# Performance work log

Hardware: AMD Instinct MI355X
Metric: run time of the kernel (lower is better)

Reference implementation:

```python
import jax, jax.numpy as jnp
import numpy as np

NUM_LEVELS = 16
FEATS_PER_LEVEL = 2
LOG2_HASHMAP = 19
TABLE_SIZE = 1 << LOG2_HASHMAP
BASE_RES = 16
DESIRED_RES = 4096
PER_LEVEL_SCALE = float(np.exp(np.log(DESIRED_RES / BASE_RES) / (NUM_LEVELS - 1)))
PRIMES = (np.uint32(1), np.uint32(2654435761), np.uint32(805459861))
N_POINTS = 2_000_000


def _level_features(x, table, level):
    # x: [N,3] in [0,1]; table: [TABLE_SIZE, F]
    scale = BASE_RES * (PER_LEVEL_SCALE ** level) - 1.0
    res = int(np.ceil(scale)) + 1
    dense = (res ** 3) <= TABLE_SIZE  # tcnn uses dense indexing when grid fits
    pos = x * scale + 0.5
    pos0 = jnp.floor(pos)
    w = pos - pos0                     # trilinear weights, [N,3]
    base = pos0.astype(jnp.uint32)
    out = jnp.zeros((x.shape[0], table.shape[1]), dtype=table.dtype)
    for c in range(8):                 # 8 corners of the voxel
        offs = [(c >> d) & 1 for d in range(3)]
        pc = [jnp.minimum(base[:, d] + np.uint32(offs[d]), np.uint32(res - 1)) for d in range(3)]
        if dense:
            idx = pc[0] + pc[1] * np.uint32(res) + pc[2] * np.uint32(res * res)
        else:
            idx = (pc[0] * PRIMES[0]) ^ (pc[1] * PRIMES[1]) ^ (pc[2] * PRIMES[2])
            idx = idx & np.uint32(TABLE_SIZE - 1)
        wt = jnp.ones(x.shape[0], dtype=x.dtype)
        for d in range(3):
            wt = wt * (w[:, d] if offs[d] else (1.0 - w[:, d]))
        out = out + wt[:, None] * table[idx.astype(jnp.int32)]
    return out


def hashgrid_encode(x, tables):
    # x: [N,3] in [0,1]; tables: [L, TABLE_SIZE, F] -> [N, L*F]
    return jnp.concatenate(
        [_level_features(x, tables[l], l) for l in range(NUM_LEVELS)], axis=-1)


def setup_inputs() -> dict:
    key = jax.random.key(0)
    k1, k2, k3, k4, k5 = jax.random.split(key, 5)
    points = jax.random.uniform(k1, (N_POINTS, 3), dtype=jnp.float32)
    # tcnn hashgrid init: uniform(-1e-4, 1e-4)
    tables = jax.random.uniform(k2, (NUM_LEVELS, TABLE_SIZE, FEATS_PER_LEVEL),
                                minval=-1e-4, maxval=1e-4, dtype=jnp.float32)
    def kaiming(k, fan_out, fan_in):
        bound = np.sqrt(2.0) * np.sqrt(3.0 / fan_in)
        return jax.random.uniform(k, (fan_out, fan_in), minval=-bound, maxval=bound,
                                  dtype=jnp.float32)
    W1 = kaiming(k3, 32, 32)
    W2 = kaiming(k4, 32, 32)
    W3 = kaiming(k5, 4, 32)
    aabb = jnp.stack([jnp.zeros(3, jnp.float32), jnp.ones(3, jnp.float32)])
    return {"points": points, "tables": tables, "W1": W1, "W2": W2, "W3": W3,
            "aabb": aabb}


def reference(points, tables, W1, W2, W3, aabb):
    texc = jnp.clip((points - aabb[0][None, :]) / (aabb[1] - aabb[0])[None, :], 0.0, 1.0)
    enc = hashgrid_encode(texc, tables)            # [N, 32]
    h = jax.nn.relu(enc @ W1.T)
    h = jax.nn.relu(h @ W2.T)
    out = h @ W3.T                                 # [N, 4]
    mn = jnp.array([0.0, 0.0, 0.0, 0.01], dtype=out.dtype)
    mx = jnp.array([1.0, 1.0, 1.0, 1.0], dtype=out.dtype)
    return jax.nn.sigmoid(out) * (mx - mn) + mn
```

## Files before the change

kernel.cpp:

```cpp
#include <hip/hip_runtime.h>
#include <cmath>


namespace {
constexpr int kLevels = 16;
constexpr unsigned kTableSize = 1u << 19;
constexpr unsigned kMask = kTableSize - 1u;
constexpr int kCells = 262144;
constexpr int kScanBlocks = 256;

typedef _Float16 half2_t __attribute__((ext_vector_type(2)));
typedef unsigned int u32;

struct LevelParams {
  float scale[kLevels];
  unsigned res[kLevels];
  int dense[kLevels];
  unsigned toff[kLevels];
  unsigned cnt[kLevels];
};
}

__global__ __launch_bounds__(256)
void conv_tables_kernel(const float2* __restrict__ src, u32* __restrict__ dst,
                        LevelParams lp,
                        const float* __restrict__ W1, const float* __restrict__ W2,
                        const float* __restrict__ W3, half2_t* __restrict__ Wh,
                        u32* __restrict__ hist0)
{
  int gid = blockIdx.x * blockDim.x + threadIdx.x;
  if (gid < 512) {
    Wh[gid] = half2_t{(_Float16)W1[2 * gid], (_Float16)W1[2 * gid + 1]};
  } else if (gid < 1024) {
    int t = gid - 512;
    Wh[512 + t] = half2_t{(_Float16)W2[2 * t], (_Float16)W2[2 * t + 1]};
  } else if (gid < 1088) {
    int t = gid - 1024;
    Wh[1024 + t] = half2_t{(_Float16)W3[2 * t], (_Float16)W3[2 * t + 1]};
  }
  if (hist0 && gid < kCells) hist0[gid] = 0u;
  int l = blockIdx.x >> 11;
  unsigned e = (unsigned)((blockIdx.x & 2047) * blockDim.x + threadIdx.x);
  if (l < kLevels && e < lp.cnt[l]) {
    float2 v = src[(size_t)l * kTableSize + e];
    dst[lp.toff[l] + e] =
        __builtin_bit_cast(u32, half2_t{(_Float16)v.x, (_Float16)v.y});
  }
}

__device__ __forceinline__ void texc_of(const float* __restrict__ pts,
                                        const float* __restrict__ aabb, int i,
                                        float& x, float& y, float& z)
{
  float a0x = aabb[0], a0y = aabb[1], a0z = aabb[2];
  float a1x = aabb[3], a1y = aabb[4], a1z = aabb[5];
  x = fminf(fmaxf((pts[3 * i + 0] - a0x) / (a1x - a0x), 0.f), 1.f);
  y = fminf(fmaxf((pts[3 * i + 1] - a0y) / (a1y - a0y), 0.f), 1.f);
  z = fminf(fmaxf((pts[3 * i + 2] - a0z) / (a1z - a0z), 0.f), 1.f);
}

__device__ __forceinline__ u32 cell_of(float x, float y, float z)
{
  int cx = min((int)(x * 64.f), 63);
  int cy = min((int)(y * 64.f), 63);
  int cz = min((int)(z * 64.f), 63);
  return (u32)(cx + (cy << 6) + (cz << 12));
}

__global__ __launch_bounds__(256)
void hist_kernel(const float* __restrict__ points, const float* __restrict__ aabb,
                 u32* __restrict__ hist, int n)
{
  int i = blockIdx.x * blockDim.x + threadIdx.x;
  if (i >= n) return;
  float x, y, z;
  texc_of(points, aabb, i, x, y, z);
  atomicAdd(&hist[cell_of(x, y, z)], 1u);
}

__global__ __launch_bounds__(1024)
void scanA_kernel(u32* __restrict__ hist, u32* __restrict__ btot)
{
  __shared__ u32 sm[1024];
  int t = threadIdx.x;
  int i = (blockIdx.x << 10) + t;
  u32 x = hist[i];
  sm[t] = x;
  __syncthreads();
  u32 v = x;
  for (int off = 1; off < 1024; off <<= 1) {
    u32 a = (t >= off) ? sm[t - off] : 0u;
    __syncthreads();
    v += a;
    sm[t] = v;
    __syncthreads();
  }
  hist[i] = v - x;
  if (t == 1023) btot[blockIdx.x] = v;
}

__global__ __launch_bounds__(256)
void scatter_kernel(const float* __restrict__ points, const float* __restrict__ aabb,
                    u32* __restrict__ hist, const u32* __restrict__ btot,
                    float4* __restrict__ sorted, u32* __restrict__ perm, int n)
{
  __shared__ u32 bb[kScanBlocks];
  int t = threadIdx.x;
  u32 xv = btot[t];
  bb[t] = xv;
  __syncthreads();
  u32 v = xv;
  for (int off = 1; off < 256; off <<= 1) {
    u32 a = (t >= off) ? bb[t - off] : 0u;
    __syncthreads();
    v += a;
    bb[t] = v;
    __syncthreads();
  }
  u32 excl = v - xv;
  __syncthreads();
  bb[t] = excl;
  __syncthreads();

  int i = blockIdx.x * 256 + t;
  if (i >= n) return;
  float x, y, z;
  texc_of(points, aabb, i, x, y, z);
  u32 c = cell_of(x, y, z);
  u32 slot = bb[c >> 10] + atomicAdd(&hist[c], 1u);
  sorted[slot] = float4{x, y, z, 0.f};
  perm[slot] = (u32)i;
}

__device__ __forceinline__ u32 sel4(uint4 v, u32 j) {
  u32 lo = (j & 1u) ? v.y : v.x;
  u32 hi = (j & 1u) ? v.w : v.z;
  return (j & 2u) ? hi : lo;
}

__device__ __forceinline__ float dot2_acc(half2_t a, half2_t b, float c) {
#if __has_builtin(__builtin_amdgcn_fdot2)
  return __builtin_amdgcn_fdot2(a, b, c, false);
#else
  return c + (float)a.x * (float)b.x + (float)a.y * (float)b.y;
#endif
}

__device__ __forceinline__ u32 encode_level(float x, float y, float z,
                                            float s, unsigned res, bool dense,
                                            const u32* __restrict__ tab)
{
  unsigned rm1 = res - 1u;
  unsigned res2 = res * res;
  float fx = x * s + 0.5f, fy = y * s + 0.5f, fz = z * s + 0.5f;
  float fx0 = floorf(fx), fy0 = floorf(fy), fz0 = floorf(fz);
  float wx = fx - fx0, wy = fy - fy0, wz = fz - fz0;
  unsigned bx = (unsigned)fx0, by = (unsigned)fy0, bz = (unsigned)fz0;
  unsigned pcx0 = min(bx, rm1), pcx1 = min(bx + 1u, rm1);

  u32 idx0[4], idx1[4];
  #pragma unroll
  for (int q = 0; q < 4; ++q) {
    unsigned oy = (unsigned)(q & 1);
    unsigned oz = (unsigned)(q >> 1);
    unsigned pcy = min(by + oy, rm1);
    unsigned pcz = min(bz + oz, rm1);
    if (dense) {
      u32 b = pcy * res + pcz * res2;
      idx0[q] = pcx0 + b;
      idx1[q] = pcx1 + b;
    } else {
      u32 h = (pcy * 2654435761u) ^ (pcz * 805459861u);
      idx0[q] = (pcx0 ^ h) & kMask;
      idx1[q] = (pcx1 ^ h) & kMask;
    }
  }
  uint4 v[4];
  #pragma unroll
  for (int q = 0; q < 4; ++q)
    v[q] = *reinterpret_cast<const uint4*>(tab + (idx0[q] & ~3u));
  u32 e1x[4] = {0u, 0u, 0u, 0u};
  #pragma unroll
  for (int q = 0; q < 4; ++q) {
    if ((idx0[q] ^ idx1[q]) >= 4u) e1x[q] = tab[idx1[q]];
  }
  float wx1 = wx, wx0 = 1.f - wx;
  float acc0 = 0.f, acc1 = 0.f;
  #pragma unroll
  for (int q = 0; q < 4; ++q) {
    unsigned oy = (unsigned)(q & 1);
    unsigned oz = (unsigned)(q >> 1);
    float wyz = (oy ? wy : 1.f - wy) * (oz ? wz : 1.f - wz);
    u32 e0 = sel4(v[q], idx0[q] & 3u);
    u32 e1g = sel4(v[q], idx1[q] & 3u);
    u32 e1 = ((idx0[q] ^ idx1[q]) < 4u) ? e1g : e1x[q];
    half2_t f0 = __builtin_bit_cast(half2_t, e0);
    half2_t f1 = __builtin_bit_cast(half2_t, e1);
    float w0 = wyz * wx0, w1 = wyz * wx1;
    acc0 += w0 * (float)f0.x + w1 * (float)f1.x;
    acc1 += w0 * (float)f0.y + w1 * (float)f1.y;
  }
  return __builtin_bit_cast(u32, half2_t{(_Float16)acc0, (_Float16)acc1});
}

__global__ __launch_bounds__(256)
void encode_dense_kernel(const float4* __restrict__ pts,
                         const u32* __restrict__ tables,
                         u32* __restrict__ enc,
                         LevelParams lp, int nd, int n)
{
  int i = blockIdx.x * blockDim.x + threadIdx.x;
  if (i >= n) return;
  float4 p = pts[i];
  #pragma unroll 1
  for (int l = 0; l < nd; ++l) {
    enc[(size_t)l * n + i] = encode_level(p.x, p.y, p.z, lp.scale[l], lp.res[l],
                                          lp.dense[l] != 0, tables + lp.toff[l]);
  }
}

__global__ __launch_bounds__(256)
void encode_level_kernel(const float4* __restrict__ pts,
                         const u32* __restrict__ tables,
                         u32* __restrict__ enc,
                         LevelParams lp, int l, int n)
{
  int i = blockIdx.x * blockDim.x + threadIdx.x;
  if (i >= n) return;
  float4 p = pts[i];
  enc[(size_t)l * n + i] = encode_level(p.x, p.y, p.z, lp.scale[l], lp.res[l],
                                        lp.dense[l] != 0, tables + lp.toff[l]);
}

__global__ __launch_bounds__(256)
void encode_raw_kernel(const float* __restrict__ points,
                       const u32* __restrict__ tables,
                       const float* __restrict__ aabb,
                       u32* __restrict__ enc,
                       LevelParams lp, int n, int bpl)
{
  int l = blockIdx.x / bpl;
  int i = (blockIdx.x - l * bpl) * blockDim.x + threadIdx.x;
  if (i >= n) return;
  float x, y, z;
  texc_of(points, aabb, i, x, y, z);
  enc[(size_t)l * n + i] = encode_level(x, y, z, lp.scale[l], lp.res[l],
                                        lp.dense[l] != 0, tables + lp.toff[l]);
}

__global__ __launch_bounds__(256)
void mlp_kernel(const u32* __restrict__ enc,
                const half2_t* __restrict__ Wh,
                const u32* __restrict__ perm,
                float* __restrict__ out, int n)
{
  int i = blockIdx.x * blockDim.x + threadIdx.x;
  if (i >= n) return;

  u32 orig = perm ? perm[i] : (u32)i;

  half2_t e[16];
  #pragma unroll
  for (int l = 0; l < kLevels; ++l)
    e[l] = __builtin_bit_cast(half2_t, enc[(size_t)l * n + i]);

  const half2_t* W1h = Wh;
  const half2_t* W2h = Wh + 512;
  const half2_t* W3h = Wh + 1024;

  half2_t h1[16];
  #pragma unroll
  for (int jj = 0; jj < 16; ++jj) {
    float a0 = 0.f, a1 = 0.f;
    #pragma unroll
    for (int k = 0; k < 16; ++k) {
      a0 = dot2_acc(e[k], W1h[16 * (2 * jj) + k], a0);
      a1 = dot2_acc(e[k], W1h[16 * (2 * jj + 1) + k], a1);
    }
    h1[jj] = half2_t{(_Float16)fmaxf(a0, 0.f), (_Float16)fmaxf(a1, 0.f)};
  }

  half2_t h2[16];
  #pragma unroll
  for (int jj = 0; jj < 16; ++jj) {
    float a0 = 0.f, a1 = 0.f;
    #pragma unroll
    for (int k = 0; k < 16; ++k) {
      a0 = dot2_acc(h1[k], W2h[16 * (2 * jj) + k], a0);
      a1 = dot2_acc(h1[k], W2h[16 * (2 * jj + 1) + k], a1);
    }
    h2[jj] = half2_t{(_Float16)fmaxf(a0, 0.f), (_Float16)fmaxf(a1, 0.f)};
  }

  float o[4];
  #pragma unroll
  for (int j = 0; j < 4; ++j) {
    float acc = 0.f;
    #pragma unroll
    for (int k = 0; k < 16; ++k) acc = dot2_acc(h2[k], W3h[16 * j + k], acc);
    o[j] = acc;
  }

  float4 r;
  r.x = 1.f / (1.f + __expf(-o[0]));
  r.y = 1.f / (1.f + __expf(-o[1]));
  r.z = 1.f / (1.f + __expf(-o[2]));
  r.w = 0.99f / (1.f + __expf(-o[3])) + 0.01f;
  reinterpret_cast<float4*>(out)[orig] = r;
}

__global__ __launch_bounds__(256)
void hashgrid_mlp_kernel(const float* __restrict__ points,
                         const float* __restrict__ tables,
                         const float* __restrict__ W1,
                         const float* __restrict__ W2,
                         const float* __restrict__ W3,
                         const float* __restrict__ aabb,
                         float* __restrict__ out,
                         LevelParams lp, int n)
{
  int i = blockIdx.x * blockDim.x + threadIdx.x;
  if (i >= n) return;
  float x, y, z;
  texc_of(points, aabb, i, x, y, z);
  float enc[2 * kLevels];
  #pragma unroll
  for (int l = 0; l < kLevels; ++l) {
    float s = lp.scale[l];
    unsigned res = lp.res[l];
    bool dense = (lp.dense[l] != 0);
    unsigned rm1 = res - 1u;
    unsigned res2 = res * res;
    float fx = x * s + 0.5f, fy = y * s + 0.5f, fz = z * s + 0.5f;
    float fx0 = floorf(fx), fy0 = floorf(fy), fz0 = floorf(fz);
    float wx = fx - fx0, wy = fy - fy0, wz = fz - fz0;
    unsigned bx = (unsigned)fx0, by = (unsigned)fy0, bz = (unsigned)fz0;
    const float2* tab = reinterpret_cast<const float2*>(tables) + (size_t)l * kTableSize;
    float acc0 = 0.f, acc1 = 0.f;
    #pragma unroll
    for (int c = 0; c < 8; ++c) {
      unsigned ox = (unsigned)(c & 1);
      unsigned oy = (unsigned)((c >> 1) & 1);
      unsigned oz = (unsigned)((c >> 2) & 1);
      unsigned pcx = min(bx + ox, rm1);
      unsigned pcy = min(by + oy, rm1);
      unsigned pcz = min(bz + oz, rm1);
      unsigned idx;
      if (dense) idx = pcx + pcy * res + pcz * res2;
      else idx = (pcx ^ (pcy * 2654435761u) ^ (pcz * 805459861u)) & kMask;
      float wt = (ox ? wx : 1.f - wx) * (oy ? wy : 1.f - wy) * (oz ? wz : 1.f - wz);
      float2 f = tab[idx];
      acc0 += wt * f.x;
      acc1 += wt * f.y;
    }
    enc[2 * l + 0] = acc0;
    enc[2 * l + 1] = acc1;
  }
  float h1[32];
  #pragma unroll
  for (int j = 0; j < 32; ++j) {
    float acc = 0.f;
    #pragma unroll
    for (int k = 0; k < 32; ++k) acc += enc[k] * W1[32 * j + k];
    h1[j] = fmaxf(acc, 0.f);
  }
  float h2[32];
  #pragma unroll
  for (int j = 0; j < 32; ++j) {
    float acc = 0.f;
    #pragma unroll
    for (int k = 0; k < 32; ++k) acc += h1[k] * W2[32 * j + k];
    h2[j] = fmaxf(acc, 0.f);
  }
  float o[4];
  #pragma unroll
  for (int j = 0; j < 4; ++j) {
    float acc = 0.f;
    #pragma unroll
    for (int k = 0; k < 32; ++k) acc += h2[k] * W3[32 * j + k];
    o[j] = acc;
  }
  float4 r;
  r.x = 1.f / (1.f + __expf(-o[0]));
  r.y = 1.f / (1.f + __expf(-o[1]));
  r.z = 1.f / (1.f + __expf(-o[2]));
  r.w = 0.99f / (1.f + __expf(-o[3])) + 0.01f;
  reinterpret_cast<float4*>(out)[i] = r;
}

extern "C" void kernel_launch(void* const* d_in, const int* in_sizes, int n_in,
                              void* d_out, int out_size, void* d_ws, size_t ws_size,
                              hipStream_t stream) {
  const float* points = (const float*)d_in[0];
  const float* tables = (const float*)d_in[1];
  const float* W1     = (const float*)d_in[2];
  const float* W2     = (const float*)d_in[3];
  const float* W3     = (const float*)d_in[4];
  const float* aabb   = (const float*)d_in[5];
  float* out = (float*)d_out;
  int n = in_sizes[0] / 3;

  LevelParams lp;
  const double pls = std::exp(std::log(4096.0 / 16.0) / 15.0);
  unsigned off = 0;
  int ndense = 0;
  for (int l = 0; l < kLevels; ++l) {
    double s = 16.0 * std::pow(pls, (double)l) - 1.0;
    lp.scale[l] = (float)s;
    long long res = (long long)std::ceil(s) + 1;
    lp.res[l] = (unsigned)res;
    long long r3 = res * res * res;
    lp.dense[l] = (r3 <= (long long)kTableSize) ? 1 : 0;
    lp.cnt[l] = lp.dense[l] ? (unsigned)r3 : kTableSize;
    lp.toff[l] = off;
    off += (lp.cnt[l] + 3u) & ~3u;
  }
  for (int l = 0; l < kLevels; ++l) { if (lp.dense[l]) ndense = l + 1; else break; }

  const int block = 256;
  const size_t tab_f16_bytes = (size_t)off * sizeof(u32);
  const size_t enc_bytes     = (size_t)kLevels * (size_t)n * sizeof(u32);
  const size_t perm_bytes    = (size_t)n * sizeof(u32);
  const size_t w_bytes       = 1088 * sizeof(half2_t);

  const size_t need_sorted = tab_f16_bytes + enc_bytes + perm_bytes + w_bytes;
  const size_t need_raw    = tab_f16_bytes + enc_bytes + w_bytes;
  const bool out_fits_scratch = (size_t)out_size >= (size_t)4 * (size_t)n;
  const bool enc_fits_hist = enc_bytes >= (size_t)(kCells + kScanBlocks) * sizeof(u32);

  const int grid_n = (n + block - 1) / block;

  if (ws_size >= need_sorted && out_fits_scratch && enc_fits_hist) {
    char* p = (char*)d_ws;
    u32*     tab_f16 = (u32*)p;                   p += tab_f16_bytes;
    u32*     enc     = (u32*)p;                   p += enc_bytes;
    u32*     perm    = (u32*)p;                   p += perm_bytes;
    half2_t* Wh      = (half2_t*)p;
    u32*     hist    = enc;
    u32*     btot    = hist + kCells;
    float4*  sorted  = (float4*)d_out;

    conv_tables_kernel<<<kLevels * 2048, block, 0, stream>>>(
        reinterpret_cast<const float2*>(tables), tab_f16, lp, W1, W2, W3, Wh, hist);
    hist_kernel<<<grid_n, block, 0, stream>>>(points, aabb, hist, n);
    scanA_kernel<<<kScanBlocks, 1024, 0, stream>>>(hist, btot);
    scatter_kernel<<<grid_n, block, 0, stream>>>(points, aabb, hist, btot,
                                                 sorted, perm, n);
    encode_dense_kernel<<<grid_n, block, 0, stream>>>(sorted, tab_f16, enc,
                                                      lp, ndense, n);
    for (int l = ndense; l < kLevels; ++l) {
      encode_level_kernel<<<grid_n, block, 0, stream>>>(sorted, tab_f16, enc,
                                                        lp, l, n);
    }
    mlp_kernel<<<grid_n, block, 0, stream>>>(enc, Wh, perm, out, n);
  } else if (ws_size >= need_raw) {
    char* p = (char*)d_ws;
    u32*     tab_f16 = (u32*)p;                   p += tab_f16_bytes;
    u32*     enc     = (u32*)p;                   p += enc_bytes;
    half2_t* Wh      = (half2_t*)p;

    const int bpl = grid_n;
    conv_tables_kernel<<<kLevels * 2048, block, 0, stream>>>(
        reinterpret_cast<const float2*>(tables), tab_f16, lp, W1, W2, W3, Wh,
        nullptr);
    encode_raw_kernel<<<bpl * kLevels, block, 0, stream>>>(
        points, tab_f16, aabb, enc, lp, n, bpl);
    mlp_kernel<<<grid_n, block, 0, stream>>>(enc, Wh, nullptr, out, n);
  } else {
    hashgrid_mlp_kernel<<<grid_n, block, 0, stream>>>(
        points, tables, W1, W2, W3, aabb, out, lp, n);
  }
}
```

Measured before the change: 843.6 us.

## Split scatter into perm-only scatter plus gather reorder; merge level encodes into one launch

The scatter kernel now writes only the permutation, and a new reorder kernel gathers points by perm so the sorted float4 array is written coalesced instead of scattered. The dense multi-level kernel and the per-level hash kernel launches are replaced by a single encode kernel whose grid covers every level, with the level taken from the block index. This removes scattered 16-byte writes and several launch gaps, at the cost of an extra kernel that does a random gather read of the points and one more pass over perm.

Measured after the change: 839.0 us. About the same (-0.6%).

```diff
diff --git a/kernel.cpp b/kernel.cpp
--- a/kernel.cpp
+++ b/kernel.cpp
@@ -100,9 +100,10 @@
 }
 
 __global__ __launch_bounds__(256)
-void scatter_kernel(const float* __restrict__ points, const float* __restrict__ aabb,
-                    u32* __restrict__ hist, const u32* __restrict__ btot,
-                    float4* __restrict__ sorted, u32* __restrict__ perm, int n)
+void scatter_perm_kernel(const float* __restrict__ points,
+                         const float* __restrict__ aabb,
+                         u32* __restrict__ hist, const u32* __restrict__ btot,
+                         u32* __restrict__ perm, int n)
 {
   __shared__ u32 bb[kScanBlocks];
   int t = threadIdx.x;
@@ -128,8 +129,21 @@
   texc_of(points, aabb, i, x, y, z);
   u32 c = cell_of(x, y, z);
   u32 slot = bb[c >> 10] + atomicAdd(&hist[c], 1u);
-  sorted[slot] = float4{x, y, z, 0.f};
   perm[slot] = (u32)i;
+}
+
+__global__ __launch_bounds__(256)
+void reorder_kernel(const float* __restrict__ points,
+                    const float* __restrict__ aabb,
+                    const u32* __restrict__ perm,
+                    float4* __restrict__ sorted, int n)
+{
+  int i = blockIdx.x * blockDim.x + threadIdx.x;
+  if (i >= n) return;
+  int orig = (int)perm[i];
+  float x, y, z;
+  texc_of(points, aabb, orig, x, y, z);
+  sorted[i] = float4{x, y, z, 0.f};
 }
 
 __device__ __forceinline__ u32 sel4(uint4 v, u32 j) {
@@ -204,28 +218,13 @@
 }
 
 __global__ __launch_bounds__(256)
-void encode_dense_kernel(const float4* __restrict__ pts,
-                         const u32* __restrict__ tables,
-                         u32* __restrict__ enc,
-                         LevelParams lp, int nd, int n)
-{
-  int i = blockIdx.x * blockDim.x + threadIdx.x;
-  if (i >= n) return;
-  float4 p = pts[i];
-  #pragma unroll 1
-  for (int l = 0; l < nd; ++l) {
-    enc[(size_t)l * n + i] = encode_level(p.x, p.y, p.z, lp.scale[l], lp.res[l],
-                                          lp.dense[l] != 0, tables + lp.toff[l]);
-  }
-}
-
-__global__ __launch_bounds__(256)
-void encode_level_kernel(const float4* __restrict__ pts,
-                         const u32* __restrict__ tables,
-                         u32* __restrict__ enc,
-                         LevelParams lp, int l, int n)
-{
-  int i = blockIdx.x * blockDim.x + threadIdx.x;
+void encode_kernel(const float4* __restrict__ pts,
+                   const u32* __restrict__ tables,
+                   u32* __restrict__ enc,
+                   LevelParams lp, int n, int bpl)
+{
+  int l = blockIdx.x / bpl;
+  int i = (blockIdx.x - l * bpl) * blockDim.x + threadIdx.x;
   if (i >= n) return;
   float4 p = pts[i];
   enc[(size_t)l * n + i] = encode_level(p.x, p.y, p.z, lp.scale[l], lp.res[l],
@@ -403,7 +402,6 @@
   LevelParams lp;
   const double pls = std::exp(std::log(4096.0 / 16.0) / 15.0);
   unsigned off = 0;
-  int ndense = 0;
   for (int l = 0; l < kLevels; ++l) {
     double s = 16.0 * std::pow(pls, (double)l) - 1.0;
     lp.scale[l] = (float)s;
@@ -415,7 +413,6 @@
     lp.toff[l] = off;
     off += (lp.cnt[l] + 3u) & ~3u;
   }
-  for (int l = 0; l < kLevels; ++l) { if (lp.dense[l]) ndense = l + 1; else break; }
 
   const int block = 256;
   const size_t tab_f16_bytes = (size_t)off * sizeof(u32);
@@ -429,6 +426,7 @@
   const bool enc_fits_hist = enc_bytes >= (size_t)(kCells + kScanBlocks) * sizeof(u32);
 
   const int grid_n = (n + block - 1) / block;
+  const int bpl = grid_n;
 
   if (ws_size >= need_sorted && out_fits_scratch && enc_fits_hist) {
     char* p = (char*)d_ws;
@@ -444,14 +442,11 @@
         reinterpret_cast<const float2*>(tables), tab_f16, lp, W1, W2, W3, Wh, hist);
     hist_kernel<<<grid_n, block, 0, stream>>>(points, aabb, hist, n);
     scanA_kernel<<<kScanBlocks, 1024, 0, stream>>>(hist, btot);
-    scatter_kernel<<<grid_n, block, 0, stream>>>(points, aabb, hist, btot,
-                                                 sorted, perm, n);
-    encode_dense_kernel<<<grid_n, block, 0, stream>>>(sorted, tab_f16, enc,
-                                                      lp, ndense, n);
-    for (int l = ndense; l < kLevels; ++l) {
-      encode_level_kernel<<<grid_n, block, 0, stream>>>(sorted, tab_f16, enc,
-                                                        lp, l, n);
-    }
+    scatter_perm_kernel<<<grid_n, block, 0, stream>>>(points, aabb, hist, btot,
+                                                      perm, n);
+    reorder_kernel<<<grid_n, block, 0, stream>>>(points, aabb, perm, sorted, n);
+    encode_kernel<<<bpl * kLevels, block, 0, stream>>>(
+        sorted, tab_f16, enc, lp, n, bpl);
     mlp_kernel<<<grid_n, block, 0, stream>>>(enc, Wh, perm, out, n);
   } else if (ws_size >= need_raw) {
     char* p = (char*)d_ws;
@@ -459,7 +454,6 @@
     u32*     enc     = (u32*)p;                   p += enc_bytes;
     half2_t* Wh      = (half2_t*)p;
 
-    const int bpl = grid_n;
     conv_tables_kernel<<<kLevels * 2048, block, 0, stream>>>(
         reinterpret_cast<const float2*>(tables), tab_f16, lp, W1, W2, W3, Wh,
         nullptr);
```
